# Kernel tuning notes

Hardware: AMD Instinct MI355X
Metric: run time of the kernel (lower is better)

Reference implementation:

```python
import jax, jax.numpy as jnp
import numpy as np

DIN = 256
T = 16                      # sample_duration
NSCALE, NRATIO = 6, 3
ANCHOR_NUM = 15             # placements of durations [16,12,8] in T=16: 1+5+9
NC_SCORE = NSCALE * NRATIO * ANCHOR_NUM * 2      # 540
NC_BBOX = NSCALE * NRATIO * ANCHOR_NUM * T * 4   # 17280
NC_SCORE16 = NSCALE * NRATIO * 2                 # 36
NC_BBOX16 = NSCALE * NRATIO * 4                  # 72
B, H, W = 4, 14, 14


def conv3d(x, w, b, padding):
    y = jax.lax.conv_general_dilated(
        x, w, window_strides=(1, 1, 1), padding=padding,
        dimension_numbers=('NCDHW', 'OIDHW', 'NCDHW'))
    return y + b[None, :, None, None, None]


def setup_inputs() -> dict:
    key = jax.random.key(0)
    ks = jax.random.split(key, 12)
    hid = DIN * 2
    s = 0.02
    return {
        'base_feat': jax.random.normal(ks[0], (B, DIN, T, H, W), jnp.float32),
        'im_info': jnp.ones((B, 3), jnp.float32) * 224.0,
        'gt_boxes': jax.random.uniform(ks[1], (B, 10, 7), jnp.float32),
        'gt_rois': jax.random.uniform(ks[2], (B, 10, 7), jnp.float32),
        'conv_w': jax.random.normal(ks[3], (hid, DIN, 3, 3, 3), jnp.float32) * s,
        'conv_b': jnp.zeros((hid,), jnp.float32),
        'cls_w': jax.random.normal(ks[4], (NC_SCORE, hid, T, 1, 1), jnp.float32) * s,
        'cls_b': jnp.zeros((NC_SCORE,), jnp.float32),
        'bbox_w': jax.random.normal(ks[5], (NC_BBOX, hid, T, 1, 1), jnp.float32) * s,
        'bbox_b': jnp.zeros((NC_BBOX,), jnp.float32),
        'cls16_w': jax.random.normal(ks[6], (NC_SCORE16, hid, T, 1, 1), jnp.float32) * s,
        'cls16_b': jnp.zeros((NC_SCORE16,), jnp.float32),
        'bbox16_w': jax.random.normal(ks[7], (NC_BBOX16, hid, T, 1, 1), jnp.float32) * s,
        'bbox16_b': jnp.zeros((NC_BBOX16,), jnp.float32),
    }


def _softmax_pairs(score, nc):
    # torch reshape2d(x,2) -> softmax(dim=1) -> reshape2d(x,nc)
    b, c, h, w = score.shape
    s = score.reshape(b, 2, (c * h) // 2, w)
    p = jax.nn.softmax(s, axis=1)
    return p.reshape(b, nc, h, w)


def reference(base_feat, im_info, gt_boxes, gt_rois,
              conv_w, conv_b, cls_w, cls_b, bbox_w, bbox_b,
              cls16_w, cls16_b, bbox16_w, bbox16_b):
    pad1 = [(1, 1), (1, 1), (1, 1)]
    rpn_conv1 = jax.nn.relu(conv3d(base_feat, conv_w, conv_b, pad1))
    # heads: kernel (T,1,1), VALID -> depth collapses to 1; squeeze(2)
    rpn_cls_score = conv3d(rpn_conv1, cls_w, cls_b, 'VALID').squeeze(2)      # [B,540,H,W]
    rpn_bbox_pred = conv3d(rpn_conv1, bbox_w, bbox_b, 'VALID').squeeze(2)    # [B,17280,H,W]
    rpn_cls_prob = _softmax_pairs(rpn_cls_score, NC_SCORE)
    rpn_cls_16 = conv3d(rpn_conv1, cls16_w, cls16_b, 'VALID').squeeze(2)     # [B,36,H,W]
    rpn_bbox_16 = conv3d(rpn_conv1, bbox16_w, bbox16_b, 'VALID').squeeze(2)  # [B,72,H,W]
    rpn_cls_prob_16 = _softmax_pairs(rpn_cls_16, NC_SCORE16)
    return (rpn_cls_prob, rpn_bbox_pred, rpn_cls_prob_16, rpn_bbox_16)
```

## Files before the change

### kernel.cpp

```cpp
#include <hip/hip_runtime.h>
#include <hip/hip_bf16.h>
#include <stdint.h>

typedef __attribute__((ext_vector_type(4))) float f32x4;
typedef __attribute__((ext_vector_type(4))) unsigned int u32x4;
typedef __bf16 v8bf __attribute__((ext_vector_type(8)));

#define GLL16(gp, lp) __builtin_amdgcn_global_load_lds( \
    (const __attribute__((address_space(1))) unsigned int*)(const void*)(gp), \
    (__attribute__((address_space(3))) unsigned int*)(void*)(lp), 16, 0, 0)

__device__ __forceinline__ unsigned pkbf(float a, float b) {
  return __builtin_amdgcn_perm(__float_as_uint(b), __float_as_uint(a), 0x07060302u);
}

#define OB1 423360
#define OB2 13970880
#define OB3 13999104

#define WS_XPAD   0
#define XPAD_GUARD_ELEMS 8192
#define WS_W1P    9519104
#define WS_X2T    16596992
#define WS_CLSS   31277056
#define WS_CLS16S 32970496
#define WS_BIAS2  33083392

__global__ void k_zero(u32x4* __restrict__ p) {
  p[blockIdx.x * 256 + threadIdx.x] = (u32x4){0u, 0u, 0u, 0u};
}

__global__ void k_fill_xpad(const float* __restrict__ bf, __hip_bfloat16* __restrict__ xp) {
  __shared__ float tile[64][65];
  int spb = blockIdx.x, cib = blockIdx.y, b = blockIdx.z;
  int t = threadIdx.x;
  int c0 = t >> 6;
  int sp_l = t & 63;
  const float* src = bf + (size_t)(b * 256 + cib * 64) * 3136 + spb * 64;
#pragma unroll
  for (int i = 0; i < 16; ++i) {
    int ci_l = i * 4 + c0;
    tile[ci_l][sp_l] = src[ci_l * 3136 + sp_l];
  }
  __syncthreads();
  int ci_l = t & 63;
#pragma unroll
  for (int i = 0; i < 16; ++i) {
    int spl = i * 4 + c0;
    int sp = spb * 64 + spl;
    int tt = sp / 196; int rr = sp - tt * 196;
    int y = rr / 14;   int x = rr - y * 14;
    int s = b * 4608 + (tt + 1) * 256 + (y + 1) * 16 + (x + 1);
    xp[(size_t)(32 + s) * 256 + cib * 64 + ci_l] = __float2bfloat16(tile[ci_l][spl]);
  }
}

__global__ void k_pack_w1(const float* __restrict__ cw, __hip_bfloat16* __restrict__ w1p) {
  int i = blockIdx.x * 256 + threadIdx.x;
  int co = i / 6912; int rem = i - co * 6912;
  int d = rem >> 8;  int ci = rem & 255;
  w1p[i] = __float2bfloat16(cw[co * 6912 + ci * 27 + d]);
}

__global__ void k_pack_bias2(const float* __restrict__ cb, const float* __restrict__ bb,
                             const float* __restrict__ c16, const float* __restrict__ b16,
                             float* __restrict__ bias2) {
  int i = blockIdx.x * 256 + threadIdx.x;
  if (i >= 18048) return;
  float v = 0.f;
  if (i < 540) v = cb[i];
  else if (i < 17820) v = bb[i - 540];
  else if (i < 17856) v = c16[i - 17820];
  else if (i < 17928) v = b16[i - 17856];
  bias2[i] = v;
}

__global__ __launch_bounds__(256, 4) void k_gemm1(
    const __hip_bfloat16* __restrict__ W1p,
    const __hip_bfloat16* __restrict__ Xp,
    const float* __restrict__ conv_b,
    __hip_bfloat16* __restrict__ X2T) {
  __shared__ short lA[64 * 64];
  __shared__ short lB[128 * 64];
  const int tid = threadIdx.x;
  const int ntile = blockIdx.x, mtile = blockIdx.y;
  const int lane = tid & 63, wave = tid >> 6;
  const int wm = wave & 1, wn = wave >> 1;

  long gA[2]; long gB[4];
#pragma unroll
  for (int i = 0; i < 2; ++i) {
    int c = i * 256 + tid;
    int row = c >> 3, pos = c & 7;
    int kc = pos ^ (row & 7);
    gA[i] = (long)(mtile * 64 + row) * 6912 + kc * 8;
  }
#pragma unroll
  for (int i = 0; i < 4; ++i) {
    int c = i * 256 + tid;
    int row = c >> 3, pos = c & 7;
    int kc = pos ^ (row & 7);
    int col = ntile * 128 + row;
    int bi = col >> 12, rem = col & 4095;
    gB[i] = (long)(bi * 4608 + rem) * 256 + kc * 8;
  }
  f32x4 acc[2][4] = {};

  for (int d = 0; d < 27; ++d) {
    int dt = d / 9; int r9 = d - dt * 9; int dy = r9 / 3; int dx = r9 - dy * 3;
    long offd = (long)(dt * 256 + (dy - 1) * 16 + (dx - 1)) * 256;
    int kd = d * 256;
    for (int ci0 = 0; ci0 < 256; ci0 += 64) {
#pragma unroll
      for (int i = 0; i < 2; ++i)
        GLL16(W1p + gA[i] + (kd + ci0), &lA[(i * 256 + tid) * 8]);
#pragma unroll
      for (int i = 0; i < 4; ++i)
        GLL16(Xp + gB[i] + offd + ci0, &lB[(i * 256 + tid) * 8]);
      __syncthreads();
#pragma unroll
      for (int ks = 0; ks < 2; ++ks) {
        v8bf af[2], bfr[4];
#pragma unroll
        for (int mi = 0; mi < 2; ++mi) {
          int row = wm * 32 + mi * 16 + (lane & 15);
          int ch = (ks * 4 + (lane >> 4)) ^ (row & 7);
          af[mi] = *(const v8bf*)&lA[row * 64 + ch * 8];
        }
#pragma unroll
        for (int ni = 0; ni < 4; ++ni) {
          int row = wn * 64 + ni * 16 + (lane & 15);
          int ch = (ks * 4 + (lane >> 4)) ^ (row & 7);
          bfr[ni] = *(const v8bf*)&lB[row * 64 + ch * 8];
        }
#pragma unroll
        for (int mi = 0; mi < 2; ++mi)
#pragma unroll
          for (int ni = 0; ni < 4; ++ni)
            acc[mi][ni] = __builtin_amdgcn_mfma_f32_16x16x32_bf16(af[mi], bfr[ni], acc[mi][ni], 0, 0, 0);
      }
      __syncthreads();
    }
  }
#pragma unroll
  for (int ni = 0; ni < 4; ++ni) {
    int col = ntile * 128 + wn * 64 + ni * 16 + (lane & 15);
    int bi = col >> 12, rem = col & 4095;
    int tt = rem >> 8, p2 = rem & 255;
    int yq = p2 >> 4, xq = p2 & 15;
    if (yq < 1 || yq > 14 || xq < 1 || xq > 14) continue;
    int n2p = bi * 208 + (yq - 1) * 14 + (xq - 1);
#pragma unroll
    for (int mi = 0; mi < 2; ++mi) {
#pragma unroll
      for (int rg = 0; rg < 4; ++rg) {
        int co = mtile * 64 + wm * 32 + mi * 16 + (lane >> 4) * 4 + rg;
        float v = acc[mi][ni][rg] + conv_b[co];
        v = fmaxf(v, 0.f);
        X2T[(size_t)n2p * 8192 + co * 16 + tt] = __float2bfloat16(v);
      }
    }
  }
}

__global__ __launch_bounds__(256, 2) void k_gemm2(
    const float* __restrict__ cls_w, const float* __restrict__ bbox_w,
    const float* __restrict__ cls16_w, const float* __restrict__ bbox16_w,
    const __hip_bfloat16* __restrict__ X2T, const float* __restrict__ bias2,
    float* __restrict__ out, float* __restrict__ cls_s, float* __restrict__ cls16_s) {
  __shared__ short lA[64 * 64];
  __shared__ short lB[416 * 64];
  const int tid = threadIdx.x;
  const int ntile = blockIdx.x, mtile = blockIdx.y;
  const int lane = tid & 63, wave = tid >> 6;
  const int wm = wave & 1, wn = wave >> 1;

  const int r = tid >> 2, q = tid & 3;
  const float* rowptr;
  {
    int o = mtile * 64 + r;
    if (o >= 17928) o = 0;
    if (o < 540) rowptr = cls_w + (size_t)o * 8192;
    else if (o < 17820) rowptr = bbox_w + (size_t)(o - 540) * 8192;
    else if (o < 17856) rowptr = cls16_w + (size_t)(o - 17820) * 8192;
    else rowptr = bbox16_w + (size_t)(o - 17856) * 8192;
    rowptr += q * 16;
  }
  const int pos0 = (q * 2) ^ (r & 7), pos1 = (q * 2 + 1) ^ (r & 7);

  long gB[13];
#pragma unroll
  for (int i = 0; i < 13; ++i) {
    int c = i * 256 + tid;
    int row = c >> 3, pos = c & 7;
    int kc = pos ^ (row & 7);
    gB[i] = (long)(ntile * 416 + row) * 8192 + kc * 8;
  }
  f32x4 acc[2][13] = {};

  float4 v0, v1, v2, v3;
  {
    const float4* p = (const float4*)rowptr;
    v0 = p[0]; v1 = p[1]; v2 = p[2]; v3 = p[3];
  }

  for (int k0 = 0; k0 < 8192; k0 += 64) {
#pragma unroll
    for (int i = 0; i < 13; ++i)
      GLL16(X2T + gB[i] + k0, &lB[(i * 256 + tid) * 8]);
    {
      u32x4 w0, w1;
      w0.x = pkbf(v0.x, v0.y); w0.y = pkbf(v0.z, v0.w);
      w0.z = pkbf(v1.x, v1.y); w0.w = pkbf(v1.z, v1.w);
      w1.x = pkbf(v2.x, v2.y); w1.y = pkbf(v2.z, v2.w);
      w1.z = pkbf(v3.x, v3.y); w1.w = pkbf(v3.z, v3.w);
      *(u32x4*)&lA[r * 64 + pos0 * 8] = w0;
      *(u32x4*)&lA[r * 64 + pos1 * 8] = w1;
    }
    if (k0 + 64 < 8192) {
      const float4* p = (const float4*)(rowptr + k0 + 64);
      v0 = p[0]; v1 = p[1]; v2 = p[2]; v3 = p[3];
    }
    __syncthreads();
#pragma unroll
    for (int ks = 0; ks < 2; ++ks) {
      v8bf af[2];
#pragma unroll
      for (int mi = 0; mi < 2; ++mi) {
        int row = wm * 32 + mi * 16 + (lane & 15);
        int ch = (ks * 4 + (lane >> 4)) ^ (row & 7);
        af[mi] = *(const v8bf*)&lA[row * 64 + ch * 8];
      }
#pragma unroll
      for (int ni = 0; ni < 13; ++ni) {
        int row = wn * 208 + ni * 16 + (lane & 15);
        int ch = (ks * 4 + (lane >> 4)) ^ (row & 7);
        v8bf bfr = *(const v8bf*)&lB[row * 64 + ch * 8];
        acc[0][ni] = __builtin_amdgcn_mfma_f32_16x16x32_bf16(af[0], bfr, acc[0][ni], 0, 0, 0);
        acc[1][ni] = __builtin_amdgcn_mfma_f32_16x16x32_bf16(af[1], bfr, acc[1][ni], 0, 0, 0);
      }
    }
    __syncthreads();
  }
  const int batch = ntile * 2 + wn;
#pragma unroll
  for (int ni = 0; ni < 13; ++ni) {
    int cib = ni * 16 + (lane & 15);
    if (cib >= 196) continue;
    int col = batch * 196 + cib;
#pragma unroll
    for (int mi = 0; mi < 2; ++mi) {
#pragma unroll
      for (int rg = 0; rg < 4; ++rg) {
        int o = mtile * 64 + wm * 32 + mi * 16 + (lane >> 4) * 4 + rg;
        if (o >= 17928) continue;
        float val = acc[mi][ni][rg] + bias2[o];
        if (o < 540) cls_s[o * 784 + col] = val;
        else if (o < 17820) out[OB1 + ((size_t)batch * 17280 + (o - 540)) * 196 + cib] = val;
        else if (o < 17856) cls16_s[(o - 17820) * 784 + col] = val;
        else out[OB3 + ((size_t)batch * 72 + (o - 17856)) * 196 + cib] = val;
      }
    }
  }
}

__global__ void k_softmax_pairs(const float* __restrict__ s, float* __restrict__ out,
                                int half, int nc, long obase) {
  int idx = blockIdx.x * 256 + threadIdx.x;
  if (idx >= half * 784) return;
  int i = idx / 784, col = idx - i * 784;
  float s0 = s[i * 784 + col];
  float s1 = s[(i + half) * 784 + col];
  float m = fmaxf(s0, s1);
  float e0 = __expf(s0 - m), e1 = __expf(s1 - m);
  float inv = 1.0f / (e0 + e1);
  int bi = col / 196, yx = col - bi * 196;
  out[obase + ((size_t)bi * nc + i) * 196 + yx] = e0 * inv;
  out[obase + ((size_t)bi * nc + i + half) * 196 + yx] = e1 * inv;
}

extern "C" void kernel_launch(void* const* d_in, const int* in_sizes, int n_in,
                              void* d_out, int out_size, void* d_ws, size_t ws_size,
                              hipStream_t stream) {
  const float* base_feat = (const float*)d_in[0];
  const float* conv_w = (const float*)d_in[4];
  const float* conv_b = (const float*)d_in[5];
  const float* cls_w = (const float*)d_in[6];
  const float* cls_b = (const float*)d_in[7];
  const float* bbox_w = (const float*)d_in[8];
  const float* bbox_b = (const float*)d_in[9];
  const float* cls16_w = (const float*)d_in[10];
  const float* cls16_b = (const float*)d_in[11];
  const float* bbox16_w = (const float*)d_in[12];
  const float* bbox16_b = (const float*)d_in[13];
  float* out = (float*)d_out;
  char* ws = (char*)d_ws;

  __hip_bfloat16* xpad = (__hip_bfloat16*)(ws + WS_XPAD);
  __hip_bfloat16* w1p = (__hip_bfloat16*)(ws + WS_W1P);
  __hip_bfloat16* x2t = (__hip_bfloat16*)(ws + WS_X2T);
  float* cls_s = (float*)(ws + WS_CLSS);
  float* cls16_s = (float*)(ws + WS_CLS16S);
  float* bias2 = (float*)(ws + WS_BIAS2);

  dim3 blk(256);
  k_zero<<<dim3(2324), blk, 0, stream>>>((u32x4*)(ws + WS_XPAD));
  k_fill_xpad<<<dim3(49, 4, 4), blk, 0, stream>>>(base_feat, xpad);
  k_pack_w1<<<dim3(13824), blk, 0, stream>>>(conv_w, w1p);
  k_pack_bias2<<<dim3(71), blk, 0, stream>>>(cls_b, bbox_b, cls16_b, bbox16_b, bias2);
  k_gemm1<<<dim3(128, 8), blk, 0, stream>>>(w1p, xpad + XPAD_GUARD_ELEMS, conv_b, x2t);
  k_gemm2<<<dim3(2, 281), blk, 0, stream>>>(cls_w, bbox_w, cls16_w, bbox16_w, x2t, bias2,
                                            out, cls_s, cls16_s);
  k_softmax_pairs<<<dim3(827), blk, 0, stream>>>(cls_s, out, 270, 540, 0L);
  k_softmax_pairs<<<dim3(56), blk, 0, stream>>>(cls16_s, out, 18, 36, (long)OB2);
}
```

Baseline: 1.484 ms.

## Double-buffer both GEMMs with explicit waitcnt pipelining and retile gemm2 per batch

The conv GEMM doubles its N tile to 256 and double-buffers LDS, so the next k-slice's global-to-LDS loads are issued before the current slice's MFMAs run, with manual vmcnt waits and raw barriers. The head GEMM switches to a 1D grid with a swizzled block order so the 4 batch tiles sharing the same weight rows run close together. It also raises the M tile to 128 rows, double-buffers the X2T tile, and prefetches two fp32 weight slices in registers. This is meant to hide memory latency and improve reuse of the large fp32 weight stream, at the cost of more LDS and registers (lower occupancy) and hand-tuned waitcnt counts that must stay matched to the issued loads.

```diff
diff --git a/kernel.cpp b/kernel.cpp
--- a/kernel.cpp
+++ b/kernel.cpp
@@ -75,76 +75,81 @@
   bias2[i] = v;
 }
 
-__global__ __launch_bounds__(256, 4) void k_gemm1(
+__global__ __launch_bounds__(256, 2) void k_gemm1(
     const __hip_bfloat16* __restrict__ W1p,
     const __hip_bfloat16* __restrict__ Xp,
     const float* __restrict__ conv_b,
     __hip_bfloat16* __restrict__ X2T) {
-  __shared__ short lA[64 * 64];
-  __shared__ short lB[128 * 64];
+  __shared__ short lds[2][(64 + 256) * 64];
   const int tid = threadIdx.x;
   const int ntile = blockIdx.x, mtile = blockIdx.y;
   const int lane = tid & 63, wave = tid >> 6;
   const int wm = wave & 1, wn = wave >> 1;
 
-  long gA[2]; long gB[4];
-#pragma unroll
-  for (int i = 0; i < 2; ++i) {
-    int c = i * 256 + tid;
-    int row = c >> 3, pos = c & 7;
-    int kc = pos ^ (row & 7);
-    gA[i] = (long)(mtile * 64 + row) * 6912 + kc * 8;
-  }
-#pragma unroll
-  for (int i = 0; i < 4; ++i) {
-    int c = i * 256 + tid;
-    int row = c >> 3, pos = c & 7;
-    int kc = pos ^ (row & 7);
-    int col = ntile * 128 + row;
-    int bi = col >> 12, rem = col & 4095;
-    gB[i] = (long)(bi * 4608 + rem) * 256 + kc * 8;
-  }
-  f32x4 acc[2][4] = {};
-
-  for (int d = 0; d < 27; ++d) {
-    int dt = d / 9; int r9 = d - dt * 9; int dy = r9 / 3; int dx = r9 - dy * 3;
-    long offd = (long)(dt * 256 + (dy - 1) * 16 + (dx - 1)) * 256;
-    int kd = d * 256;
-    for (int ci0 = 0; ci0 < 256; ci0 += 64) {
-#pragma unroll
-      for (int i = 0; i < 2; ++i)
-        GLL16(W1p + gA[i] + (kd + ci0), &lA[(i * 256 + tid) * 8]);
-#pragma unroll
-      for (int i = 0; i < 4; ++i)
-        GLL16(Xp + gB[i] + offd + ci0, &lB[(i * 256 + tid) * 8]);
-      __syncthreads();
+  const int srow = tid >> 3;
+  const int kc8 = ((tid & 7) ^ (srow & 7)) * 8;
+  const long gA0 = (long)(mtile * 64 + srow) * 6912 + kc8;
+  const long gB0 = (long)((ntile >> 4) * 4608 + (ntile & 15) * 256 + srow) * 256 + kc8;
+
+  f32x4 acc[2][8] = {};
+
+  auto issue1 = [&](int it2, int buf2) {
+    int d = it2 >> 2, ci0 = (it2 & 3) << 6;
+    int dt = d / 9, r9 = d - dt * 9;
+    int dy = r9 / 3, dx = r9 - dy * 3;
+    long offA = d * 256 + ci0;
+    long offB = (long)(dt * 256 + (dy - 1) * 16 + (dx - 1)) * 256 + ci0;
+    short* la = &lds[buf2][0];
+    short* lb = &lds[buf2][4096];
+#pragma unroll
+    for (int i = 0; i < 2; ++i)
+      GLL16(W1p + gA0 + (long)i * 221184 + offA, &la[(i * 256 + tid) * 8]);
+#pragma unroll
+    for (int i = 0; i < 8; ++i)
+      GLL16(Xp + gB0 + (long)i * 8192 + offB, &lb[(i * 256 + tid) * 8]);
+  };
+
+  issue1(0, 0);
+#pragma unroll 1
+  for (int it = 0; it < 108; ++it) {
+    const int buf = it & 1;
+    if (it + 1 < 108) {
+      issue1(it + 1, buf ^ 1);
+      asm volatile("s_waitcnt vmcnt(10)" ::: "memory");
+    } else {
+      asm volatile("s_waitcnt vmcnt(0)" ::: "memory");
+    }
+    __builtin_amdgcn_s_barrier();
+    __builtin_amdgcn_sched_barrier(0);
+    {
+      const short* la = &lds[buf][0];
+      const short* lb = &lds[buf][4096];
 #pragma unroll
       for (int ks = 0; ks < 2; ++ks) {
-        v8bf af[2], bfr[4];
+        v8bf af[2];
 #pragma unroll
         for (int mi = 0; mi < 2; ++mi) {
           int row = wm * 32 + mi * 16 + (lane & 15);
           int ch = (ks * 4 + (lane >> 4)) ^ (row & 7);
-          af[mi] = *(const v8bf*)&lA[row * 64 + ch * 8];
+          af[mi] = *(const v8bf*)&la[row * 64 + ch * 8];
         }
 #pragma unroll
-        for (int ni = 0; ni < 4; ++ni) {
-          int row = wn * 64 + ni * 16 + (lane & 15);
+        for (int ni = 0; ni < 8; ++ni) {
+          int row = wn * 128 + ni * 16 + (lane & 15);
           int ch = (ks * 4 + (lane >> 4)) ^ (row & 7);
-          bfr[ni] = *(const v8bf*)&lB[row * 64 + ch * 8];
+          v8bf bfr = *(const v8bf*)&lb[row * 64 + ch * 8];
+          acc[0][ni] = __builtin_amdgcn_mfma_f32_16x16x32_bf16(af[0], bfr, acc[0][ni], 0, 0, 0);
+          acc[1][ni] = __builtin_amdgcn_mfma_f32_16x16x32_bf16(af[1], bfr, acc[1][ni], 0, 0, 0);
         }
-#pragma unroll
-        for (int mi = 0; mi < 2; ++mi)
-#pragma unroll
-          for (int ni = 0; ni < 4; ++ni)
-            acc[mi][ni] = __builtin_amdgcn_mfma_f32_16x16x32_bf16(af[mi], bfr[ni], acc[mi][ni], 0, 0, 0);
-      }
-      __syncthreads();
-    }
-  }
-#pragma unroll
-  for (int ni = 0; ni < 4; ++ni) {
-    int col = ntile * 128 + wn * 64 + ni * 16 + (lane & 15);
+      }
+    }
+    __builtin_amdgcn_sched_barrier(0);
+    __builtin_amdgcn_s_barrier();
+  }
+
+#pragma unroll
+  for (int ni = 0; ni < 8; ++ni) {
+    int col = ntile * 256 + wn * 128 + ni * 16 + (lane & 15);
     int bi = col >> 12, rem = col & 4095;
     int tt = rem >> 8, p2 = rem & 255;
     int yq = p2 >> 4, xq = p2 & 15;
@@ -168,97 +173,119 @@
     const float* __restrict__ cls16_w, const float* __restrict__ bbox16_w,
     const __hip_bfloat16* __restrict__ X2T, const float* __restrict__ bias2,
     float* __restrict__ out, float* __restrict__ cls_s, float* __restrict__ cls16_s) {
-  __shared__ short lA[64 * 64];
-  __shared__ short lB[416 * 64];
+  __shared__ short lA[128 * 64];
+  __shared__ short lB[2][224 * 64];
   const int tid = threadIdx.x;
-  const int ntile = blockIdx.x, mtile = blockIdx.y;
-  const int lane = tid & 63, wave = tid >> 6;
-  const int wm = wave & 1, wn = wave >> 1;
-
-  const int r = tid >> 2, q = tid & 3;
+  const int wsl = (int)(blockIdx.x & 7) * 72 + (int)(blockIdx.x >> 3);
+  const int mtile = wsl >> 2, ntile = wsl & 3;
+  if (mtile >= 141) return;
+  const int lane = tid & 63, wm = tid >> 6;
+
+  const int r = tid >> 1, h = tid & 1;
   const float* rowptr;
   {
-    int o = mtile * 64 + r;
+    int o = mtile * 128 + r;
     if (o >= 17928) o = 0;
     if (o < 540) rowptr = cls_w + (size_t)o * 8192;
     else if (o < 17820) rowptr = bbox_w + (size_t)(o - 540) * 8192;
     else if (o < 17856) rowptr = cls16_w + (size_t)(o - 17820) * 8192;
     else rowptr = bbox16_w + (size_t)(o - 17856) * 8192;
-    rowptr += q * 16;
-  }
-  const int pos0 = (q * 2) ^ (r & 7), pos1 = (q * 2 + 1) ^ (r & 7);
-
-  long gB[13];
-#pragma unroll
-  for (int i = 0; i < 13; ++i) {
-    int c = i * 256 + tid;
-    int row = c >> 3, pos = c & 7;
-    int kc = pos ^ (row & 7);
-    gB[i] = (long)(ntile * 416 + row) * 8192 + kc * 8;
-  }
+    rowptr += h * 32;
+  }
+  const long gB0 = (long)(ntile * 208 + (tid >> 3)) * 8192 +
+                   (long)(((tid & 7) ^ ((tid >> 3) & 7)) * 8);
+
   f32x4 acc[2][13] = {};
-
-  float4 v0, v1, v2, v3;
-  {
-    const float4* p = (const float4*)rowptr;
-    v0 = p[0]; v1 = p[1]; v2 = p[2]; v3 = p[3];
-  }
-
-  for (int k0 = 0; k0 < 8192; k0 += 64) {
-#pragma unroll
-    for (int i = 0; i < 13; ++i)
-      GLL16(X2T + gB[i] + k0, &lB[(i * 256 + tid) * 8]);
-    {
-      u32x4 w0, w1;
-      w0.x = pkbf(v0.x, v0.y); w0.y = pkbf(v0.z, v0.w);
-      w0.z = pkbf(v1.x, v1.y); w0.w = pkbf(v1.z, v1.w);
-      w1.x = pkbf(v2.x, v2.y); w1.y = pkbf(v2.z, v2.w);
-      w1.z = pkbf(v3.x, v3.y); w1.w = pkbf(v3.z, v3.w);
-      *(u32x4*)&lA[r * 64 + pos0 * 8] = w0;
-      *(u32x4*)&lA[r * 64 + pos1 * 8] = w1;
-    }
-    if (k0 + 64 < 8192) {
-      const float4* p = (const float4*)(rowptr + k0 + 64);
-      v0 = p[0]; v1 = p[1]; v2 = p[2]; v3 = p[3];
-    }
-    __syncthreads();
+  float4 vaA[8], vaB[8];
+
+  auto loadA = [&](float4* va, int k0) {
+    const float4* p = (const float4*)(rowptr + k0);
+#pragma unroll
+    for (int j = 0; j < 8; ++j) va[j] = p[j];
+  };
+  auto stageA = [&](const float4* va) {
+#pragma unroll
+    for (int j = 0; j < 4; ++j) {
+      u32x4 wv;
+      wv.x = pkbf(va[2 * j].x, va[2 * j].y);
+      wv.y = pkbf(va[2 * j].z, va[2 * j].w);
+      wv.z = pkbf(va[2 * j + 1].x, va[2 * j + 1].y);
+      wv.w = pkbf(va[2 * j + 1].z, va[2 * j + 1].w);
+      int pj = (h * 4 + j) ^ (r & 7);
+      *(u32x4*)&lA[r * 64 + pj * 8] = wv;
+    }
+  };
+  auto issueB = [&](int step, int bufb) {
+    long off = (long)step * 64;
+#pragma unroll
+    for (int i = 0; i < 7; ++i)
+      GLL16(X2T + gB0 + (long)i * 262144 + off, &lB[bufb][(i * 256 + tid) * 8]);
+  };
+  auto mfmaPhase = [&](int bufb) {
 #pragma unroll
     for (int ks = 0; ks < 2; ++ks) {
-      v8bf af[2];
-#pragma unroll
-      for (int mi = 0; mi < 2; ++mi) {
-        int row = wm * 32 + mi * 16 + (lane & 15);
+      v8bf af0, af1;
+      {
+        int row0 = wm * 32 + (lane & 15);
+        int ch0 = (ks * 4 + (lane >> 4)) ^ (row0 & 7);
+        af0 = *(const v8bf*)&lA[row0 * 64 + ch0 * 8];
+        af1 = *(const v8bf*)&lA[(row0 + 16) * 64 + ch0 * 8];
+      }
+#pragma unroll
+      for (int ni = 0; ni < 13; ++ni) {
+        int row = ni * 16 + (lane & 15);
         int ch = (ks * 4 + (lane >> 4)) ^ (row & 7);
-        af[mi] = *(const v8bf*)&lA[row * 64 + ch * 8];
-      }
-#pragma unroll
-      for (int ni = 0; ni < 13; ++ni) {
-        int row = wn * 208 + ni * 16 + (lane & 15);
-        int ch = (ks * 4 + (lane >> 4)) ^ (row & 7);
-        v8bf bfr = *(const v8bf*)&lB[row * 64 + ch * 8];
-        acc[0][ni] = __builtin_amdgcn_mfma_f32_16x16x32_bf16(af[0], bfr, acc[0][ni], 0, 0, 0);
-        acc[1][ni] = __builtin_amdgcn_mfma_f32_16x16x32_bf16(af[1], bfr, acc[1][ni], 0, 0, 0);
-      }
-    }
-    __syncthreads();
-  }
-  const int batch = ntile * 2 + wn;
+        v8bf bfr = *(const v8bf*)&lB[bufb][row * 64 + ch * 8];
+        acc[0][ni] = __builtin_amdgcn_mfma_f32_16x16x32_bf16(af0, bfr, acc[0][ni], 0, 0, 0);
+        acc[1][ni] = __builtin_amdgcn_mfma_f32_16x16x32_bf16(af1, bfr, acc[1][ni], 0, 0, 0);
+      }
+    }
+  };
+
+  issueB(0, 0);
+  loadA(vaA, 0);
+  loadA(vaB, 64);
+
+#pragma unroll 1
+  for (int it = 0; it < 128; it += 2) {
+    stageA(vaA);
+    issueB(it + 1, 1);
+    if (it + 2 < 128) loadA(vaA, (it + 2) * 64);
+    if (it < 126) asm volatile("s_waitcnt vmcnt(23) lgkmcnt(0)" ::: "memory");
+    else          asm volatile("s_waitcnt vmcnt(15) lgkmcnt(0)" ::: "memory");
+    __builtin_amdgcn_s_barrier();
+    __builtin_amdgcn_sched_barrier(0);
+    mfmaPhase(0);
+    __builtin_amdgcn_sched_barrier(0);
+    __builtin_amdgcn_s_barrier();
+    stageA(vaB);
+    if (it + 2 < 128) issueB(it + 2, 0);
+    if (it + 3 < 128) loadA(vaB, (it + 3) * 64);
+    if (it < 126) asm volatile("s_waitcnt vmcnt(23) lgkmcnt(0)" ::: "memory");
+    else          asm volatile("s_waitcnt vmcnt(0) lgkmcnt(0)" ::: "memory");
+    __builtin_amdgcn_s_barrier();
+    __builtin_amdgcn_sched_barrier(0);
+    mfmaPhase(1);
+    __builtin_amdgcn_sched_barrier(0);
+    __builtin_amdgcn_s_barrier();
+  }
+
 #pragma unroll
   for (int ni = 0; ni < 13; ++ni) {
     int cib = ni * 16 + (lane & 15);
     if (cib >= 196) continue;
-    int col = batch * 196 + cib;
+    int col = ntile * 196 + cib;
 #pragma unroll
     for (int mi = 0; mi < 2; ++mi) {
 #pragma unroll
       for (int rg = 0; rg < 4; ++rg) {
-        int o = mtile * 64 + wm * 32 + mi * 16 + (lane >> 4) * 4 + rg;
+        int o = mtile * 128 + wm * 32 + mi * 16 + (lane >> 4) * 4 + rg;
         if (o >= 17928) continue;
         float val = acc[mi][ni][rg] + bias2[o];
         if (o < 540) cls_s[o * 784 + col] = val;
-        else if (o < 17820) out[OB1 + ((size_t)batch * 17280 + (o - 540)) * 196 + cib] = val;
+        else if (o < 17820) out[OB1 + ((size_t)ntile * 17280 + (o - 540)) * 196 + cib] = val;
         else if (o < 17856) cls16_s[(o - 17820) * 784 + col] = val;
-        else out[OB3 + ((size_t)batch * 72 + (o - 17856)) * 196 + cib] = val;
+        else out[OB3 + ((size_t)ntile * 72 + (o - 17856)) * 196 + cib] = val;
       }
     }
   }
@@ -308,9 +335,9 @@
   k_fill_xpad<<<dim3(49, 4, 4), blk, 0, stream>>>(base_feat, xpad);
   k_pack_w1<<<dim3(13824), blk, 0, stream>>>(conv_w, w1p);
   k_pack_bias2<<<dim3(71), blk, 0, stream>>>(cls_b, bbox_b, cls16_b, bbox16_b, bias2);
-  k_gemm1<<<dim3(128, 8), blk, 0, stream>>>(w1p, xpad + XPAD_GUARD_ELEMS, conv_b, x2t);
-  k_gemm2<<<dim3(2, 281), blk, 0, stream>>>(cls_w, bbox_w, cls16_w, bbox16_w, x2t, bias2,
-                                            out, cls_s, cls16_s);
+  k_gemm1<<<dim3(64, 8), blk, 0, stream>>>(w1p, xpad + XPAD_GUARD_ELEMS, conv_b, x2t);
+  k_gemm2<<<dim3(576), blk, 0, stream>>>(cls_w, bbox_w, cls16_w, bbox16_w, x2t, bias2,
+                                         out, cls_s, cls16_s);
   k_softmax_pairs<<<dim3(827), blk, 0, stream>>>(cls_s, out, 270, 540, 0L);
   k_softmax_pairs<<<dim3(56), blk, 0, stream>>>(cls16_s, out, 18, 36, (long)OB2);
 }
```

After: 1.416 ms. 1.05x faster.
